# Kernel optimization log

Measured on AMD Instinct MI355X. Metric: run time of the kernel, lower is better.

Reference implementation:

```python
import jax, jax.numpy as jnp
import numpy as np
import math

B, S, HID, H, WBAND = 2, 4096, 768, 12, 128
D = HID // H  # 64


def _band_qk(q, k, w):
    """q,k: [B,S,H,D] -> banded scores [B,S,H,2w+1] (offset d -> key pos i+d-w)."""
    b, s, h, d = q.shape
    nc = s // w
    kp = jnp.pad(k, ((0, 0), (w, w), (0, 0), (0, 0)))  # zero padding_value
    idx = (jnp.arange(nc) * w)[:, None] + jnp.arange(3 * w)[None, :]  # [nc,3w]
    kw = kp[:, idx]                                   # [B,nc,3w,H,D]
    qc = q.reshape(b, nc, w, h, d)
    scores = jnp.einsum('bcxhd,bcyhd->bchxy', qc, kw)  # [B,nc,H,w,3w]
    # extract diagonals: P[x,dd] = scores[x, x+dd] via flatten/skew trick
    flat = scores.reshape(b, nc, h, w * 3 * w)
    flat = jnp.pad(flat, ((0, 0), (0, 0), (0, 0), (0, w)))
    diag = flat.reshape(b, nc, h, w, 3 * w + 1)[..., : 2 * w + 1]
    return diag.transpose(0, 1, 3, 2, 4).reshape(b, s, h, 2 * w + 1)


def _band_pv(p, v, w):
    """p: [B,S,H,2w+1], v: [B,S,H,D] -> context [B,S,H,D]."""
    b, s, h, k = p.shape
    d = v.shape[-1]
    nc = s // w
    vp = jnp.pad(v, ((0, 0), (w, w), (0, 0), (0, 0)))
    idx = (jnp.arange(nc) * w)[:, None] + jnp.arange(3 * w)[None, :]
    vw = vp[:, idx]                                   # [B,nc,3w,H,D]
    pc = p.reshape(b, nc, w, h, k).transpose(0, 1, 3, 2, 4)  # [B,nc,H,w,2w+1]
    pc = jnp.pad(pc, ((0, 0), (0, 0), (0, 0), (0, 0), (0, w)))  # [..,w,3w+1]
    band = pc.reshape(b, nc, h, w * (3 * w + 1))[..., : w * 3 * w]
    band = band.reshape(b, nc, h, w, 3 * w)           # M[x, x+dd] = p[x,dd]
    ctx = jnp.einsum('bchxy,bcyhd->bcxhd', band, vw)  # [B,nc,w,H,D]
    return ctx.reshape(b, s, h, d)


def setup_inputs() -> dict:
    key = jax.random.key(0)
    ks = jax.random.split(key, 8)
    init = lambda k, shp: (jax.random.normal(k, shp, jnp.float32) * 0.02)
    return {
        'x': jax.random.normal(ks[0], (B, S, HID), jnp.float32),
        'Wq': init(ks[1], (HID, HID)), 'bq': jnp.zeros((HID,), jnp.float32),
        'Wk': init(ks[2], (HID, HID)), 'bk': jnp.zeros((HID,), jnp.float32),
        'Wv': init(ks[3], (HID, HID)), 'bv': jnp.zeros((HID,), jnp.float32),
        'Wd': init(ks[4], (H, D, HID)), 'bd': jnp.zeros((HID,), jnp.float32),
        'gamma': jnp.ones((HID,), jnp.float32),
        'beta': jnp.zeros((HID,), jnp.float32),
    }


def reference(x, Wq, bq, Wk, bk, Wv, bv, Wd, bd, gamma, beta):
    w = WBAND
    b, s, _ = x.shape
    q = (x @ Wq + bq).reshape(b, s, H, D) / math.sqrt(D)
    k = (x @ Wk + bk).reshape(b, s, H, D)
    v = (x @ Wv + bv).reshape(b, s, H, D)
    scores = _band_qk(q, k, w)                        # [B,S,H,2w+1]
    # mask_invalid_locations: key pos i + d - w must lie in [0, S)
    pos = jnp.arange(s)[:, None] + jnp.arange(2 * w + 1)[None, :] - w
    valid = (pos >= 0) & (pos < s)                    # [S,2w+1]
    scores = jnp.where(valid[None, :, None, :], scores, -1e9)
    probs = jax.nn.softmax(scores, axis=-1)           # float32 softmax
    ctx = _band_pv(probs, v, w)                       # [B,S,H,D]
    proj = jnp.einsum('bfnd,ndh->bfh', ctx, Wd) + bd  # output projection
    y = x + proj                                      # residual (dropout=0)
    mu = jnp.mean(y, axis=-1, keepdims=True)
    var = jnp.mean(jnp.square(y - mu), axis=-1, keepdims=True)
    out = (y - mu) / jnp.sqrt(var + 1e-12) * gamma + beta
    return out
```

## Files before the change

### kernel.cpp

```cpp
#include <hip/hip_runtime.h>
#include <math.h>

typedef unsigned short u16;
typedef __bf16 bf16x8 __attribute__((ext_vector_type(8)));
typedef float f32x4 __attribute__((ext_vector_type(4)));

constexpr int Bc   = 2;
constexpr int Sc   = 4096;
constexpr int HIDc = 768;
constexpr int Hc   = 12;
constexpr int Dc   = 64;
constexpr int Wc   = 128;
constexpr int Mc   = Bc * Sc;

constexpr int QT3  = 128;
constexpr int WIN3 = 384;
constexpr int NCT3 = 18;

#define VM_BAR(N) asm volatile("s_waitcnt vmcnt(" #N ")\n\ts_barrier" ::: "memory")
#define BAR()     asm volatile("s_barrier" ::: "memory")

static __device__ __forceinline__ void load_lds16(const void* g, void* l) {
    __builtin_amdgcn_global_load_lds(
        (const __attribute__((address_space(1))) void*)g,
        (__attribute__((address_space(3))) void*)l, 16, 0, 0);
}
static __device__ __forceinline__ u16 to_bf16(float f) {
    return __builtin_bit_cast(u16, (__bf16)f);
}

__global__ __launch_bounds__(256) void prep_x(const float* __restrict__ x,
                                              u16* __restrict__ xb,
                                              u16* __restrict__ zpad)
{
    int i = blockIdx.x * 256 + threadIdx.x;
    float4 v = ((const float4*)x)[i];
    ushort4 o;
    o.x = to_bf16(v.x); o.y = to_bf16(v.y);
    o.z = to_bf16(v.z); o.w = to_bf16(v.w);
    ((ushort4*)xb)[i] = o;
    if (blockIdx.x == 0 && threadIdx.x < 128)
        ((int4*)zpad)[threadIdx.x] = make_int4(0, 0, 0, 0);
}

__global__ __launch_bounds__(256) void prep_w(
    const float* __restrict__ Wq, const float* __restrict__ Wk,
    const float* __restrict__ Wv, const float* __restrict__ Wd,
    u16* __restrict__ wqt, u16* __restrict__ wkt,
    u16* __restrict__ wvt, u16* __restrict__ wdt)
{
    const int z = blockIdx.z;
    const float* W = z == 0 ? Wq : z == 1 ? Wk : z == 2 ? Wv : Wd;
    u16* T         = z == 0 ? wqt : z == 1 ? wkt : z == 2 ? wvt : wdt;

    __shared__ float t[32][33];
    const int bx = blockIdx.x * 32, by = blockIdx.y * 32;
    const int tx = threadIdx.x & 31, ty = threadIdx.x >> 5;
#pragma unroll
    for (int i = 0; i < 32; i += 8)
        t[ty + i][tx] = W[(size_t)(by + ty + i) * HIDc + bx + tx];
    __syncthreads();
#pragma unroll
    for (int i = 0; i < 32; i += 8)
        T[(size_t)(bx + ty + i) * HIDc + by + tx] = to_bf16(t[tx][ty + i]);
}

__device__ __forceinline__ void stage64(const u16* __restrict__ A,
                                        const u16* __restrict__ Bt,
                                        int m0, int n0, int k0,
                                        u16* As, u16* Bs, int soff)
{
#pragma unroll
    for (int i = 0; i < 4; ++i) {
        int off  = soff + i * 1024;
        int row  = off >> 7;
        int slot = (off >> 4) & 7;
        int seg  = slot ^ (row & 7);
        load_lds16(A  + (size_t)(m0 + row) * HIDc + k0 + seg * 8, (char*)As + off);
        load_lds16(Bt + (size_t)(n0 + row) * HIDc + k0 + seg * 8, (char*)Bs + off);
    }
}

template <int SWAP>
__device__ __forceinline__ void gemm128_core(
    const u16* __restrict__ A, const u16* __restrict__ Bt,
    int m0, int n0, u16* As, u16* Bs, f32x4 (&acc)[4][4])
{
    const int lane = threadIdx.x & 63, wid = threadIdx.x >> 6;
    const int c16 = lane & 15, g = lane >> 4;
    const int wm = (wid >> 1) * 64, wn = (wid & 1) * 64;
    const int soff = wid * 4096 + lane * 16;

    stage64(A, Bt, m0, n0, 0, As, Bs, soff);
    int cur = 0;
    for (int t = 0; t < 12; ++t) {
        if (t < 11) {
            stage64(A, Bt, m0, n0, (t + 1) * 64,
                    As + (cur ^ 1) * 8192, Bs + (cur ^ 1) * 8192, soff);
            VM_BAR(8);
        } else {
            VM_BAR(0);
        }
        const u16* Ab = As + cur * 8192;
        const u16* Bb = Bs + cur * 8192;
#pragma unroll
        for (int kk = 0; kk < 2; ++kk) {
            bf16x8 af[4], bfr[4];
#pragma unroll
            for (int tt = 0; tt < 4; ++tt) {
                int ar = wm + tt * 16 + c16;
                int a8 = (kk * 4 + g) ^ (ar & 7);
                af[tt] = *(const bf16x8*)(Ab + ar * 64 + a8 * 8);
                int br = wn + tt * 16 + c16;
                int b8 = (kk * 4 + g) ^ (br & 7);
                bfr[tt] = *(const bf16x8*)(Bb + br * 64 + b8 * 8);
            }
            __builtin_amdgcn_s_setprio(1);
#pragma unroll
            for (int mt = 0; mt < 4; ++mt)
#pragma unroll
                for (int nt = 0; nt < 4; ++nt)
                    acc[mt][nt] = SWAP
                        ? __builtin_amdgcn_mfma_f32_16x16x32_bf16(
                              bfr[nt], af[mt], acc[mt][nt], 0, 0, 0)
                        : __builtin_amdgcn_mfma_f32_16x16x32_bf16(
                              af[mt], bfr[nt], acc[mt][nt], 0, 0, 0);
            __builtin_amdgcn_s_setprio(0);
        }
        BAR();
        cur ^= 1;
    }
}

__global__ __launch_bounds__(256) void gemm_qk_mfma(
    const u16* __restrict__ xb,
    const u16* __restrict__ wqt, const u16* __restrict__ wkt,
    const float* __restrict__ bq, const float* __restrict__ bk,
    u16* __restrict__ qg, u16* __restrict__ kg)
{
    __shared__ u16 As[16384], Bs[16384];
    const int z = blockIdx.z;
    const u16* Bt     = z ? wkt : wqt;
    const float* bias = z ? bk : bq;
    const float scale = z ? 1.0f : 0.125f;
    u16* outp         = z ? kg : qg;

    const int m0 = blockIdx.x * 128, n0 = blockIdx.y * 128;
    f32x4 acc[4][4];
#pragma unroll
    for (int i = 0; i < 4; ++i)
#pragma unroll
        for (int j = 0; j < 4; ++j) acc[i][j] = (f32x4){0.f, 0.f, 0.f, 0.f};

    gemm128_core<1>(xb, Bt, m0, n0, As, Bs, acc);

    const int lane = threadIdx.x & 63, wid = threadIdx.x >> 6;
    const int c16 = lane & 15, g = lane >> 4;
    const int wm = (wid >> 1) * 64, wn = (wid & 1) * 64;

#pragma unroll
    for (int mt = 0; mt < 4; ++mt) {
        int m = m0 + wm + mt * 16 + c16;
        int b = m >> 12, s = m & (Sc - 1);
        size_t rowbase = (size_t)(b * Hc) * Sc * Dc + (size_t)s * Dc;
#pragma unroll
        for (int nt = 0; nt < 4; ++nt) {
            int nb = n0 + wn + nt * 16 + g * 4;
            int h = nb >> 6, d0 = nb & 63;
            float4 b4 = *(const float4*)&bias[nb];
            ushort4 pk;
            pk.x = to_bf16((acc[mt][nt][0] + b4.x) * scale);
            pk.y = to_bf16((acc[mt][nt][1] + b4.y) * scale);
            pk.z = to_bf16((acc[mt][nt][2] + b4.z) * scale);
            pk.w = to_bf16((acc[mt][nt][3] + b4.w) * scale);
            *(ushort4*)&outp[rowbase + (size_t)h * Sc * Dc + d0] = pk;
        }
    }
}

__global__ __launch_bounds__(256) void gemm_v_mfma(
    const u16* __restrict__ xb, const u16* __restrict__ wvt,
    const float* __restrict__ bv, u16* __restrict__ vtg)
{
    __shared__ u16 As[16384], Bs[16384];
    const int m0 = blockIdx.x * 128, n0 = blockIdx.y * 128;
    f32x4 acc[4][4];
#pragma unroll
    for (int i = 0; i < 4; ++i)
#pragma unroll
        for (int j = 0; j < 4; ++j) acc[i][j] = (f32x4){0.f, 0.f, 0.f, 0.f};

    gemm128_core<0>(xb, wvt, m0, n0, As, Bs, acc);

    const int lane = threadIdx.x & 63, wid = threadIdx.x >> 6;
    const int c16 = lane & 15, g = lane >> 4;
    const int wm = (wid >> 1) * 64, wn = (wid & 1) * 64;

#pragma unroll
    for (int nt = 0; nt < 4; ++nt) {
        int n = n0 + wn + nt * 16 + c16;
        int h = n >> 6, d = n & 63;
        float bn = bv[n];
#pragma unroll
        for (int mt = 0; mt < 4; ++mt) {
            int m = m0 + wm + mt * 16 + g * 4;
            int b = m >> 12, s = m & (Sc - 1);
            size_t base = ((size_t)(b * Hc + h)) * Sc * Dc + (size_t)d * Sc + s;
            ushort4 pk;
            pk.x = to_bf16(acc[mt][nt][0] + bn);
            pk.y = to_bf16(acc[mt][nt][1] + bn);
            pk.z = to_bf16(acc[mt][nt][2] + bn);
            pk.w = to_bf16(acc[mt][nt][3] + bn);
            *(ushort4*)&vtg[base] = pk;
        }
    }
}

__global__ __launch_bounds__(256) void gemm_proj_mfma(
    const u16* __restrict__ ctxb, const u16* __restrict__ wdt,
    const float* __restrict__ bd, const float* __restrict__ x,
    float* __restrict__ y)
{
    __shared__ u16 As[16384], Bs[16384];
    const int m0 = blockIdx.x * 128, n0 = blockIdx.y * 128;
    f32x4 acc[4][4];
#pragma unroll
    for (int i = 0; i < 4; ++i)
#pragma unroll
        for (int j = 0; j < 4; ++j) acc[i][j] = (f32x4){0.f, 0.f, 0.f, 0.f};

    gemm128_core<1>(ctxb, wdt, m0, n0, As, Bs, acc);

    const int lane = threadIdx.x & 63, wid = threadIdx.x >> 6;
    const int c16 = lane & 15, g = lane >> 4;
    const int wm = (wid >> 1) * 64, wn = (wid & 1) * 64;

#pragma unroll
    for (int mt = 0; mt < 4; ++mt) {
        int m = m0 + wm + mt * 16 + c16;
#pragma unroll
        for (int nt = 0; nt < 4; ++nt) {
            int nb = n0 + wn + nt * 16 + g * 4;
            float4 b4 = *(const float4*)&bd[nb];
            float4 x4 = *(const float4*)&x[(size_t)m * HIDc + nb];
            float4 o4;
            o4.x = acc[mt][nt][0] + b4.x + x4.x;
            o4.y = acc[mt][nt][1] + b4.y + x4.y;
            o4.z = acc[mt][nt][2] + b4.z + x4.z;
            o4.w = acc[mt][nt][3] + b4.w + x4.w;
            *(float4*)&y[(size_t)m * HIDc + nb] = o4;
        }
    }
}

__global__ __launch_bounds__(512) void band_attn_mfma(
    const u16* __restrict__ qg, const u16* __restrict__ kg,
    const u16* __restrict__ vtg, const u16* __restrict__ zpad,
    u16* __restrict__ ctxb)
{
    extern __shared__ u16 sm[];
    u16* kwin = sm;
    u16* vt   = sm + 24576;
    u16* pm   = sm;

    const int L = blockIdx.x;
    const int xcd = L & 7, tt = L >> 3;
    const int hb = xcd * 3 + (tt % 3);
    const int qc = tt / 3;
    const int h = hb % Hc, b = hb / Hc;

    const int s0 = qc * QT3;
    const int tid = threadIdx.x;
    const int lane = tid & 63, w = tid >> 6;
    const int c16 = lane & 15, g = lane >> 4;
    const size_t hbase = ((size_t)(b * Hc + h)) * Sc * Dc;

    const u16* qp = &qg[hbase + (size_t)(s0 + w * 16 + c16) * Dc + g * 8];
    bf16x8 qa0 = *(const bf16x8*)qp;
    bf16x8 qa1 = *(const bf16x8*)(qp + 32);

#pragma unroll
    for (int i = 0; i < 6; ++i) {
        int c   = i * 8 + w;
        int row = c * 8 + (lane >> 3);
        int seg = (lane & 7) ^ (lane >> 3);
        int pos = s0 - Wc + row;
        const u16* src = (pos >= 0 && pos < Sc)
                       ? &kg[hbase + (size_t)pos * Dc + seg * 8] : zpad;
        load_lds16(src, (char*)kwin + c * 1024 + (lane & 63) * 16);
    }
#pragma unroll
    for (int i = 0; i < 6; ++i) {
        int c   = i * 8 + w;
        int idx = c * 64 + lane;
        int d   = idx / 48;
        int p   = idx - d * 48;
        int seg = (p & ~7) | ((p ^ d) & 7);
        int pos0 = s0 - Wc + seg * 8;
        const u16* src = (pos0 >= 0 && pos0 < Sc)
                       ? &vtg[hbase + (size_t)d * Sc + pos0] : zpad;
        load_lds16(src, (char*)vt + idx * 16);
    }

    VM_BAR(6);

    const int tb  = w & ~1;
    const int off = (w & 1) * 16;
    f32x4 acc[NCT3];
#pragma unroll
    for (int ct = 0; ct < NCT3; ++ct) acc[ct] = (f32x4){0.f, 0.f, 0.f, 0.f};
    __builtin_amdgcn_s_setprio(1);
#pragma unroll
    for (int ct = 0; ct < NCT3; ++ct) {
        int row = (tb + ct) * 16 + c16;
        const u16* kb = kwin + row * 64;
        bf16x8 kb0 = *(const bf16x8*)(kb + (g       ^ (row & 7)) * 8);
        bf16x8 kb1 = *(const bf16x8*)(kb + ((g + 4) ^ (row & 7)) * 8);
        acc[ct] = __builtin_amdgcn_mfma_f32_16x16x32_bf16(qa0, kb0, acc[ct], 0, 0, 0);
        acc[ct] = __builtin_amdgcn_mfma_f32_16x16x32_bf16(qa1, kb1, acc[ct], 0, 0, 0);
    }
    __builtin_amdgcn_s_setprio(0);

    float mrow[4] = {-3e38f, -3e38f, -3e38f, -3e38f};
#pragma unroll
    for (int ct = 0; ct < NCT3; ++ct) {
#pragma unroll
        for (int r = 0; r < 4; ++r) {
            int ql  = g * 4 + r;
            int jl  = ct * 16 + c16 - off;
            int pos = s0 - Wc + (tb + ct) * 16 + c16;
            bool valid = (jl >= ql) && (jl <= ql + 2 * Wc) && (pos >= 0) && (pos < Sc);
            float v = valid ? acc[ct][r] : -3e38f;
            acc[ct][r] = v;
            mrow[r] = fmaxf(mrow[r], v);
        }
    }
#pragma unroll
    for (int r = 0; r < 4; ++r)
#pragma unroll
        for (int o2 = 1; o2 < 16; o2 <<= 1)
            mrow[r] = fmaxf(mrow[r], __shfl_xor(mrow[r], o2));

    float srow[4] = {0.f, 0.f, 0.f, 0.f};
#pragma unroll
    for (int ct = 0; ct < NCT3; ++ct)
#pragma unroll
        for (int r = 0; r < 4; ++r) {
            float e = __expf(acc[ct][r] - mrow[r]);
            acc[ct][r] = e;
            srow[r] += e;
        }
#pragma unroll
    for (int r = 0; r < 4; ++r)
#pragma unroll
        for (int o2 = 1; o2 < 16; o2 <<= 1)
            srow[r] += __shfl_xor(srow[r], o2);

    VM_BAR(0);

    float sq0 = __shfl(srow[0], (c16 >> 2) << 4);
    float sq1 = __shfl(srow[1], (c16 >> 2) << 4);
    float sq2 = __shfl(srow[2], (c16 >> 2) << 4);
    float sq3 = __shfl(srow[3], (c16 >> 2) << 4);
    int rr = c16 & 3;
    float sq = rr == 0 ? sq0 : rr == 1 ? sq1 : rr == 2 ? sq2 : sq3;
    float invq = 1.f / sq;

    const int qrow = w * 16 + c16;
    f32x4 o[4];
#pragma unroll
    for (int dt = 0; dt < 4; ++dt) o[dt] = (f32x4){0.f, 0.f, 0.f, 0.f};

#pragma unroll
    for (int ct = 0; ct < 10; ++ct)
#pragma unroll
        for (int r = 0; r < 4; ++r) {
            int q   = w * 16 + g * 4 + r;
            int col = ct * 16 + c16;
            int sl  = col >> 3;
            int ph  = (sl & ~7) | ((sl ^ q ^ (q >> 3)) & 7);
            pm[q * 192 + ph * 8 + (col & 7)] = to_bf16(acc[ct][r]);
        }
    __builtin_amdgcn_s_setprio(1);
#pragma unroll
    for (int ks = 0; ks < 5; ++ks) {
        int sl = ks * 4 + g;
        int ph = (sl & ~7) | ((sl ^ qrow ^ (qrow >> 3)) & 7);
        bf16x8 pa = *(const bf16x8*)(pm + qrow * 192 + ph * 8);
#pragma unroll
        for (int dt = 0; dt < 4; ++dt) {
            int d  = dt * 16 + c16;
            int vs = tb * 2 + ks * 4 + g;
            int pv = (vs & ~7) | ((vs ^ d) & 7);
            bf16x8 vb = *(const bf16x8*)(vt + d * 384 + pv * 8);
            o[dt] = __builtin_amdgcn_mfma_f32_16x16x32_bf16(vb, pa, o[dt], 0, 0, 0);
        }
    }
    __builtin_amdgcn_s_setprio(0);

#pragma unroll
    for (int ct = 10; ct < NCT3; ++ct)
#pragma unroll
        for (int r = 0; r < 4; ++r) {
            int q   = w * 16 + g * 4 + r;
            int col = ct * 16 + c16 - 160;
            int sl  = col >> 3;
            int ph  = (sl & ~7) | ((sl ^ q ^ (q >> 3)) & 7);
            pm[q * 192 + ph * 8 + (col & 7)] = to_bf16(acc[ct][r]);
        }
    __builtin_amdgcn_s_setprio(1);
#pragma unroll
    for (int ks = 0; ks < 4; ++ks) {
        int sl = ks * 4 + g;
        int ph = (sl & ~7) | ((sl ^ qrow ^ (qrow >> 3)) & 7);
        bf16x8 pa = *(const bf16x8*)(pm + qrow * 192 + ph * 8);
#pragma unroll
        for (int dt = 0; dt < 4; ++dt) {
            int d  = dt * 16 + c16;
            int vs = tb * 2 + 20 + ks * 4 + g;
            int pv = (vs & ~7) | ((vs ^ d) & 7);
            bf16x8 vb = *(const bf16x8*)(vt + d * 384 + pv * 8);
            o[dt] = __builtin_amdgcn_mfma_f32_16x16x32_bf16(vb, pa, o[dt], 0, 0, 0);
        }
    }
    __builtin_amdgcn_s_setprio(0);

    const size_t crow = ((size_t)(b * Sc + s0 + qrow)) * HIDc + h * Dc;
#pragma unroll
    for (int dt = 0; dt < 4; ++dt) {
        ushort4 pk;
        pk.x = to_bf16(o[dt][0] * invq);
        pk.y = to_bf16(o[dt][1] * invq);
        pk.z = to_bf16(o[dt][2] * invq);
        pk.w = to_bf16(o[dt][3] * invq);
        *(ushort4*)&ctxb[crow + dt * 16 + g * 4] = pk;
    }
}

__global__ __launch_bounds__(256) void ln_kernel(
    const float* __restrict__ y,
    const float* __restrict__ gamma, const float* __restrict__ beta,
    float* __restrict__ out)
{
    const int m = blockIdx.x;
    const float* row = y + (size_t)m * HIDc;
    const int t = threadIdx.x;
    float v0 = row[t], v1 = row[t + 256], v2 = row[t + 512];
    float s = v0 + v1 + v2;
    __shared__ float red[4];
    const int lane = t & 63, wid = t >> 6;
#pragma unroll
    for (int o = 1; o < 64; o <<= 1) s += __shfl_xor(s, o);
    if (lane == 0) red[wid] = s;
    __syncthreads();
    const float mu = (red[0] + red[1] + red[2] + red[3]) * (1.f / HIDc);
    v0 -= mu; v1 -= mu; v2 -= mu;
    float s2 = v0 * v0 + v1 * v1 + v2 * v2;
#pragma unroll
    for (int o = 1; o < 64; o <<= 1) s2 += __shfl_xor(s2, o);
    __syncthreads();
    if (lane == 0) red[wid] = s2;
    __syncthreads();
    const float var = (red[0] + red[1] + red[2] + red[3]) * (1.f / HIDc);
    const float rstd = rsqrtf(var + 1e-12f);
    const size_t base = (size_t)m * HIDc;
    out[base + t]       = v0 * rstd * gamma[t]       + beta[t];
    out[base + t + 256] = v1 * rstd * gamma[t + 256] + beta[t + 256];
    out[base + t + 512] = v2 * rstd * gamma[t + 512] + beta[t + 512];
}

extern "C" void kernel_launch(void* const* d_in, const int* in_sizes, int n_in,
                              void* d_out, int out_size, void* d_ws, size_t ws_size,
                              hipStream_t stream)
{
    const float* x     = (const float*)d_in[0];
    const float* Wq    = (const float*)d_in[1];
    const float* bq    = (const float*)d_in[2];
    const float* Wk    = (const float*)d_in[3];
    const float* bk    = (const float*)d_in[4];
    const float* Wv    = (const float*)d_in[5];
    const float* bv    = (const float*)d_in[6];
    const float* Wd    = (const float*)d_in[7];
    const float* bd    = (const float*)d_in[8];
    const float* gamma = (const float*)d_in[9];
    const float* beta  = (const float*)d_in[10];
    float* out = (float*)d_out;

    constexpr size_t CHUNK = (size_t)Mc * HIDc;
    constexpr size_t WSZ   = (size_t)HIDc * HIDc;
    u16* xb   = (u16*)d_ws;
    u16* wqt  = xb + CHUNK;
    u16* wkt  = wqt + WSZ;
    u16* wvt  = wkt + WSZ;
    u16* wdt  = wvt + WSZ;
    u16* qg   = wdt + WSZ;
    u16* kg   = qg + CHUNK;
    u16* vtg  = kg + CHUNK;
    u16* ctxb = vtg + CHUNK;
    float* yws = (float*)(ctxb + CHUNK);
    u16* zpad  = (u16*)(yws + CHUNK);

    prep_x<<<(CHUNK / 4) / 256, 256, 0, stream>>>(x, xb, zpad);
    prep_w<<<dim3(24, 24, 4), 256, 0, stream>>>(Wq, Wk, Wv, Wd, wqt, wkt, wvt, wdt);

    gemm_qk_mfma<<<dim3(Mc / 128, HIDc / 128, 2), 256, 0, stream>>>(
        xb, wqt, wkt, bq, bk, qg, kg);
    gemm_v_mfma<<<dim3(Mc / 128, HIDc / 128), 256, 0, stream>>>(
        xb, wvt, bv, vtg);

    band_attn_mfma<<<dim3(Sc / QT3 * Hc * Bc), 512, 98304, stream>>>(
        qg, kg, vtg, zpad, ctxb);

    gemm_proj_mfma<<<dim3(Mc / 128, HIDc / 128), 256, 0, stream>>>(
        ctxb, wdt, bd, x, yws);

    ln_kernel<<<Mc, 256, 0, stream>>>(yws, gamma, beta, out);
}
```

Baseline: 127.2 us.

## Merge Q/K/V GEMMs into one launch and shrink K-tile to 32

The Q/K and V projection GEMMs are combined into a single kernel launch with a third grid z-slice that picks the V weight and its transposed output layout. The GEMM core now stages 32-wide K slices with a new paired-row XOR swizzle instead of 64-wide ones, halving LDS per block (32KB instead of 64KB), which may allow more resident blocks per CU. The trade-off is twice as many loop iterations and barriers per tile. The merged launch also removes one kernel boundary and lets the V tiles overlap with the Q/K tiles.

```diff
diff --git a/kernel.cpp b/kernel.cpp
--- a/kernel.cpp
+++ b/kernel.cpp
@@ -14,7 +14,6 @@
 constexpr int Mc   = Bc * Sc;
 
 constexpr int QT3  = 128;
-constexpr int WIN3 = 384;
 constexpr int NCT3 = 18;
 
 #define VM_BAR(N) asm volatile("s_waitcnt vmcnt(" #N ")\n\ts_barrier" ::: "memory")
@@ -65,85 +64,82 @@
         T[(size_t)(bx + ty + i) * HIDc + by + tx] = to_bf16(t[tx][ty + i]);
 }
 
-__device__ __forceinline__ void stage64(const u16* __restrict__ A,
-                                        const u16* __restrict__ Bt,
-                                        int m0, int n0, int k0,
-                                        u16* As, u16* Bs, int soff)
-{
-#pragma unroll
-    for (int i = 0; i < 4; ++i) {
-        int off  = soff + i * 1024;
-        int row  = off >> 7;
-        int slot = (off >> 4) & 7;
-        int seg  = slot ^ (row & 7);
-        load_lds16(A  + (size_t)(m0 + row) * HIDc + k0 + seg * 8, (char*)As + off);
-        load_lds16(Bt + (size_t)(n0 + row) * HIDc + k0 + seg * 8, (char*)Bs + off);
+__device__ __forceinline__ void stage32(const u16* __restrict__ M,
+                                        int r0, int k0, u16* lds)
+{
+    const int tid = threadIdx.x;
+#pragma unroll
+    for (int i = 0; i < 2; ++i) {
+        int u    = tid + i * 256;
+        int pair = u >> 3, phys = u & 7;
+        int s8   = phys ^ (pair & 7);
+        int row  = 2 * pair + (s8 >> 2);
+        int kseg = s8 & 3;
+        load_lds16(M + (size_t)(r0 + row) * HIDc + k0 + kseg * 8,
+                   (char*)lds + u * 16);
     }
 }
 
 template <int SWAP>
-__device__ __forceinline__ void gemm128_core(
+__device__ __forceinline__ void gemm128_core32(
     const u16* __restrict__ A, const u16* __restrict__ Bt,
     int m0, int n0, u16* As, u16* Bs, f32x4 (&acc)[4][4])
 {
     const int lane = threadIdx.x & 63, wid = threadIdx.x >> 6;
     const int c16 = lane & 15, g = lane >> 4;
     const int wm = (wid >> 1) * 64, wn = (wid & 1) * 64;
-    const int soff = wid * 4096 + lane * 16;
-
-    stage64(A, Bt, m0, n0, 0, As, Bs, soff);
+
+    stage32(A,  m0, 0, As);
+    stage32(Bt, n0, 0, Bs);
     int cur = 0;
-    for (int t = 0; t < 12; ++t) {
-        if (t < 11) {
-            stage64(A, Bt, m0, n0, (t + 1) * 64,
-                    As + (cur ^ 1) * 8192, Bs + (cur ^ 1) * 8192, soff);
-            VM_BAR(8);
+    for (int t = 0; t < 24; ++t) {
+        if (t < 23) {
+            stage32(A,  m0, (t + 1) * 32, As + (cur ^ 1) * 4096);
+            stage32(Bt, n0, (t + 1) * 32, Bs + (cur ^ 1) * 4096);
+            VM_BAR(4);
         } else {
             VM_BAR(0);
         }
-        const u16* Ab = As + cur * 8192;
-        const u16* Bb = Bs + cur * 8192;
-#pragma unroll
-        for (int kk = 0; kk < 2; ++kk) {
-            bf16x8 af[4], bfr[4];
-#pragma unroll
-            for (int tt = 0; tt < 4; ++tt) {
-                int ar = wm + tt * 16 + c16;
-                int a8 = (kk * 4 + g) ^ (ar & 7);
-                af[tt] = *(const bf16x8*)(Ab + ar * 64 + a8 * 8);
-                int br = wn + tt * 16 + c16;
-                int b8 = (kk * 4 + g) ^ (br & 7);
-                bfr[tt] = *(const bf16x8*)(Bb + br * 64 + b8 * 8);
-            }
-            __builtin_amdgcn_s_setprio(1);
-#pragma unroll
-            for (int mt = 0; mt < 4; ++mt)
-#pragma unroll
-                for (int nt = 0; nt < 4; ++nt)
-                    acc[mt][nt] = SWAP
-                        ? __builtin_amdgcn_mfma_f32_16x16x32_bf16(
-                              bfr[nt], af[mt], acc[mt][nt], 0, 0, 0)
-                        : __builtin_amdgcn_mfma_f32_16x16x32_bf16(
-                              af[mt], bfr[nt], acc[mt][nt], 0, 0, 0);
-            __builtin_amdgcn_s_setprio(0);
-        }
+        const u16* Ab = As + cur * 4096;
+        const u16* Bb = Bs + cur * 4096;
+        bf16x8 af[4], bfr[4];
+#pragma unroll
+        for (int tt = 0; tt < 4; ++tt) {
+            int ar = wm + tt * 16 + c16;
+            int ap = ar >> 1, a8 = (((ar & 1) << 2) | g) ^ (ap & 7);
+            af[tt] = *(const bf16x8*)(Ab + ap * 64 + a8 * 8);
+            int br = wn + tt * 16 + c16;
+            int bp = br >> 1, b8 = (((br & 1) << 2) | g) ^ (bp & 7);
+            bfr[tt] = *(const bf16x8*)(Bb + bp * 64 + b8 * 8);
+        }
+        __builtin_amdgcn_s_setprio(1);
+#pragma unroll
+        for (int mt = 0; mt < 4; ++mt)
+#pragma unroll
+            for (int nt = 0; nt < 4; ++nt)
+                acc[mt][nt] = SWAP
+                    ? __builtin_amdgcn_mfma_f32_16x16x32_bf16(
+                          bfr[nt], af[mt], acc[mt][nt], 0, 0, 0)
+                    : __builtin_amdgcn_mfma_f32_16x16x32_bf16(
+                          af[mt], bfr[nt], acc[mt][nt], 0, 0, 0);
+        __builtin_amdgcn_s_setprio(0);
         BAR();
         cur ^= 1;
     }
 }
 
-__global__ __launch_bounds__(256) void gemm_qk_mfma(
+__global__ __launch_bounds__(256) void gemm_qkv_mfma(
     const u16* __restrict__ xb,
     const u16* __restrict__ wqt, const u16* __restrict__ wkt,
+    const u16* __restrict__ wvt,
     const float* __restrict__ bq, const float* __restrict__ bk,
-    u16* __restrict__ qg, u16* __restrict__ kg)
-{
-    __shared__ u16 As[16384], Bs[16384];
+    const float* __restrict__ bv,
+    u16* __restrict__ qg, u16* __restrict__ kg, u16* __restrict__ vtg)
+{
+    __shared__ u16 As[8192], Bs[8192];
     const int z = blockIdx.z;
-    const u16* Bt     = z ? wkt : wqt;
-    const float* bias = z ? bk : bq;
-    const float scale = z ? 1.0f : 0.125f;
-    u16* outp         = z ? kg : qg;
+    const u16* Bt     = z == 0 ? wqt : z == 1 ? wkt : wvt;
+    const float* bias = z == 0 ? bq : z == 1 ? bk : bv;
 
     const int m0 = blockIdx.x * 128, n0 = blockIdx.y * 128;
     f32x4 acc[4][4];
@@ -151,67 +147,52 @@
     for (int i = 0; i < 4; ++i)
 #pragma unroll
         for (int j = 0; j < 4; ++j) acc[i][j] = (f32x4){0.f, 0.f, 0.f, 0.f};
-
-    gemm128_core<1>(xb, Bt, m0, n0, As, Bs, acc);
 
     const int lane = threadIdx.x & 63, wid = threadIdx.x >> 6;
     const int c16 = lane & 15, g = lane >> 4;
     const int wm = (wid >> 1) * 64, wn = (wid & 1) * 64;
 
-#pragma unroll
-    for (int mt = 0; mt < 4; ++mt) {
-        int m = m0 + wm + mt * 16 + c16;
-        int b = m >> 12, s = m & (Sc - 1);
-        size_t rowbase = (size_t)(b * Hc) * Sc * Dc + (size_t)s * Dc;
+    if (z == 2) {
+        gemm128_core32<0>(xb, Bt, m0, n0, As, Bs, acc);
 #pragma unroll
         for (int nt = 0; nt < 4; ++nt) {
-            int nb = n0 + wn + nt * 16 + g * 4;
-            int h = nb >> 6, d0 = nb & 63;
-            float4 b4 = *(const float4*)&bias[nb];
-            ushort4 pk;
-            pk.x = to_bf16((acc[mt][nt][0] + b4.x) * scale);
-            pk.y = to_bf16((acc[mt][nt][1] + b4.y) * scale);
-            pk.z = to_bf16((acc[mt][nt][2] + b4.z) * scale);
-            pk.w = to_bf16((acc[mt][nt][3] + b4.w) * scale);
-            *(ushort4*)&outp[rowbase + (size_t)h * Sc * Dc + d0] = pk;
-        }
-    }
-}
-
-__global__ __launch_bounds__(256) void gemm_v_mfma(
-    const u16* __restrict__ xb, const u16* __restrict__ wvt,
-    const float* __restrict__ bv, u16* __restrict__ vtg)
-{
-    __shared__ u16 As[16384], Bs[16384];
-    const int m0 = blockIdx.x * 128, n0 = blockIdx.y * 128;
-    f32x4 acc[4][4];
-#pragma unroll
-    for (int i = 0; i < 4; ++i)
-#pragma unroll
-        for (int j = 0; j < 4; ++j) acc[i][j] = (f32x4){0.f, 0.f, 0.f, 0.f};
-
-    gemm128_core<0>(xb, wvt, m0, n0, As, Bs, acc);
-
-    const int lane = threadIdx.x & 63, wid = threadIdx.x >> 6;
-    const int c16 = lane & 15, g = lane >> 4;
-    const int wm = (wid >> 1) * 64, wn = (wid & 1) * 64;
-
-#pragma unroll
-    for (int nt = 0; nt < 4; ++nt) {
-        int n = n0 + wn + nt * 16 + c16;
-        int h = n >> 6, d = n & 63;
-        float bn = bv[n];
+            int n = n0 + wn + nt * 16 + c16;
+            int h = n >> 6, d = n & 63;
+            float bn = bias[n];
+#pragma unroll
+            for (int mt = 0; mt < 4; ++mt) {
+                int m = m0 + wm + mt * 16 + g * 4;
+                int b = m >> 12, s = m & (Sc - 1);
+                size_t base = ((size_t)(b * Hc + h)) * Sc * Dc + (size_t)d * Sc + s;
+                ushort4 pk;
+                pk.x = to_bf16(acc[mt][nt][0] + bn);
+                pk.y = to_bf16(acc[mt][nt][1] + bn);
+                pk.z = to_bf16(acc[mt][nt][2] + bn);
+                pk.w = to_bf16(acc[mt][nt][3] + bn);
+                *(ushort4*)&vtg[base] = pk;
+            }
+        }
+    } else {
+        gemm128_core32<1>(xb, Bt, m0, n0, As, Bs, acc);
+        const float scale = z ? 1.0f : 0.125f;
+        u16* outp = z ? kg : qg;
 #pragma unroll
         for (int mt = 0; mt < 4; ++mt) {
-            int m = m0 + wm + mt * 16 + g * 4;
+            int m = m0 + wm + mt * 16 + c16;
             int b = m >> 12, s = m & (Sc - 1);
-            size_t base = ((size_t)(b * Hc + h)) * Sc * Dc + (size_t)d * Sc + s;
-            ushort4 pk;
-            pk.x = to_bf16(acc[mt][nt][0] + bn);
-            pk.y = to_bf16(acc[mt][nt][1] + bn);
-            pk.z = to_bf16(acc[mt][nt][2] + bn);
-            pk.w = to_bf16(acc[mt][nt][3] + bn);
-            *(ushort4*)&vtg[base] = pk;
+            size_t rowbase = (size_t)(b * Hc) * Sc * Dc + (size_t)s * Dc;
+#pragma unroll
+            for (int nt = 0; nt < 4; ++nt) {
+                int nb = n0 + wn + nt * 16 + g * 4;
+                int h = nb >> 6, d0 = nb & 63;
+                float4 b4 = *(const float4*)&bias[nb];
+                ushort4 pk;
+                pk.x = to_bf16((acc[mt][nt][0] + b4.x) * scale);
+                pk.y = to_bf16((acc[mt][nt][1] + b4.y) * scale);
+                pk.z = to_bf16((acc[mt][nt][2] + b4.z) * scale);
+                pk.w = to_bf16((acc[mt][nt][3] + b4.w) * scale);
+                *(ushort4*)&outp[rowbase + (size_t)h * Sc * Dc + d0] = pk;
+            }
         }
     }
 }
@@ -221,7 +202,7 @@
     const float* __restrict__ bd, const float* __restrict__ x,
     float* __restrict__ y)
 {
-    __shared__ u16 As[16384], Bs[16384];
+    __shared__ u16 As[8192], Bs[8192];
     const int m0 = blockIdx.x * 128, n0 = blockIdx.y * 128;
     f32x4 acc[4][4];
 #pragma unroll
@@ -229,7 +210,7 @@
 #pragma unroll
         for (int j = 0; j < 4; ++j) acc[i][j] = (f32x4){0.f, 0.f, 0.f, 0.f};
 
-    gemm128_core<1>(ctxb, wdt, m0, n0, As, Bs, acc);
+    gemm128_core32<1>(ctxb, wdt, m0, n0, As, Bs, acc);
 
     const int lane = threadIdx.x & 63, wid = threadIdx.x >> 6;
     const int c16 = lane & 15, g = lane >> 4;
@@ -503,10 +484,8 @@
     prep_x<<<(CHUNK / 4) / 256, 256, 0, stream>>>(x, xb, zpad);
     prep_w<<<dim3(24, 24, 4), 256, 0, stream>>>(Wq, Wk, Wv, Wd, wqt, wkt, wvt, wdt);
 
-    gemm_qk_mfma<<<dim3(Mc / 128, HIDc / 128, 2), 256, 0, stream>>>(
-        xb, wqt, wkt, bq, bk, qg, kg);
-    gemm_v_mfma<<<dim3(Mc / 128, HIDc / 128), 256, 0, stream>>>(
-        xb, wvt, bv, vtg);
+    gemm_qkv_mfma<<<dim3(Mc / 128, HIDc / 128, 3), 256, 0, stream>>>(
+        xb, wqt, wkt, wvt, bq, bk, bv, qg, kg, vtg);
 
     band_attn_mfma<<<dim3(Sc / QT3 * Hc * Bc), 512, 98304, stream>>>(
         qg, kg, vtg, zpad, ctxb);
```

Measured after the change: 146.2 us. 1.15x slower.
